# Kernel optimization log

Hardware: AMD Instinct MI355X
Metric: run time of the kernel (lower is better)

## Reference

```python
import jax, jax.numpy as jnp
import numpy as np

WINDOW = 5  # window_size
HALF = WINDOW // 2


def setup_inputs() -> dict:
    key = jax.random.key(0)
    k_x, k_w1, k_w2, k_b2 = jax.random.split(key, 4)
    N, D, D1, D2 = 200000, 320, 10, 5
    x = jax.random.normal(k_x, (N, D), dtype=jnp.float32)
    # torch Linear default init ~ U(-1/sqrt(fan_in), 1/sqrt(fan_in))
    W1 = jax.random.uniform(k_w1, (D1, D), dtype=jnp.float32, minval=-1, maxval=1) / np.sqrt(D)
    W2 = jax.random.uniform(k_w2, (D2, D1), dtype=jnp.float32, minval=-1, maxval=1) / np.sqrt(D1)
    b2 = jax.random.uniform(k_b2, (D2,), dtype=jnp.float32, minval=-1, maxval=1) / np.sqrt(D1)
    return {"x": x, "W1": W1, "W2": W2, "b2": b2}


def reference(x, W1, W2, b2):
    # linear1 (no bias) -> relu  (dropout is identity at inference)
    h = jax.nn.relu(x @ W1.T)                      # [N, dim1]
    # linear2 (+bias) -> (dropout identity) -> relu
    t = jax.nn.relu(h @ W2.T + b2)                 # [N, dim2]
    N, C = t.shape
    # zero-padded sliding window of size 5 over rows, fused gather
    padded = jnp.pad(t, ((HALF, HALF), (0, 0)))    # [N+4, C]
    win = jnp.stack([padded[k:k + N] for k in range(WINDOW)], axis=1)  # [N, 5, C]
    return win.reshape(N, WINDOW * C)              # [N, 25]
```

## Files before the change

### kernel.cpp

```cpp
#include <hip/hip_runtime.h>

#define D4    80
#define DIM1  10
#define DIM2  5
#define BLK   256
#define RPI   8
#define ITERS 10
#define CROWS (RPI * ITERS)
#define OROWS (CROWS - 4)

typedef float __attribute__((ext_vector_type(4))) f32x4;

__device__ __forceinline__ float row16_sum(float v) {
    int p;
    p = __builtin_amdgcn_update_dpp(0, __float_as_int(v), 0x128, 0xF, 0xF, true);
    v += __int_as_float(p);
    p = __builtin_amdgcn_update_dpp(0, __float_as_int(v), 0x124, 0xF, 0xF, true);
    v += __int_as_float(p);
    p = __builtin_amdgcn_update_dpp(0, __float_as_int(v), 0x122, 0xF, 0xF, true);
    v += __int_as_float(p);
    p = __builtin_amdgcn_update_dpp(0, __float_as_int(v), 0x121, 0xF, 0xF, true);
    v += __int_as_float(p);
    return v;
}

__global__ __launch_bounds__(BLK, 2)
void fused_fcl_win(const f32x4* __restrict__ x4,
                   const f32x4* __restrict__ w1g,
                   const float* __restrict__ w2,
                   const float* __restrict__ b2,
                   float*       __restrict__ out,
                   int N)
{
    __shared__ float t_lds[CROWS * DIM2];

    const int tid  = threadIdx.x;
    const int lane = tid & 63;
    const int wave = tid >> 6;
    const int s    = lane & 15;
    const int half = (lane >> 4) & 1;
    const int slot = wave * 2 + (lane >> 5);

    f32x4 w1r[5][5];
    {
        const f32x4* wp = w1g + (half * 5) * D4 + s;
        #pragma unroll
        for (int dd = 0; dd < 5; ++dd)
            #pragma unroll
            for (int i = 0; i < 5; ++i)
                w1r[dd][i] = wp[dd * D4 + i * 16];
    }

    const int j = (s < DIM2) ? s : 0;
    float w2h[5];
    #pragma unroll
    for (int dd = 0; dd < 5; ++dd)
        w2h[dd] = w2[j * DIM1 + half * 5 + dd];
    const float b2r = b2[j];

    const int base = (int)blockIdx.x * OROWS;

    auto loadrow = [&](int it, f32x4* xv) {
        int r  = base - 2 + it * RPI + slot;
        int rc = min(max(r, 0), N - 1);
        const f32x4* xp = x4 + (size_t)rc * D4 + s;
        #pragma unroll
        for (int i = 0; i < 5; ++i)
            xv[i] = __builtin_nontemporal_load(xp + i * 16);
    };

    f32x4 xv[5];
    loadrow(0, xv);

    for (int it = 0; it < ITERS; ++it) {
        f32x4 xn[5];
        if (it + 1 < ITERS) loadrow(it + 1, xn);

        float partial = 0.f;
        #pragma unroll
        for (int dd = 0; dd < 5; ++dd) {
            float acc = 0.f;
            #pragma unroll
            for (int i = 0; i < 5; ++i) {
                f32x4 a  = w1r[dd][i];
                f32x4 xx = xv[i];
                acc += xx.x * a.x; acc += xx.y * a.y;
                acc += xx.z * a.z; acc += xx.w * a.w;
            }
            acc = row16_sum(acc);
            partial += fmaxf(acc, 0.f) * w2h[dd];
        }
        const float other = __shfl_xor(partial, 16);
        float t5 = fmaxf(b2r + partial + other, 0.f);

        const int r = base - 2 + it * RPI + slot;
        if (r < 0 || r >= N) t5 = 0.f;
        if (half == 0 && s < DIM2)
            t_lds[(it * RPI + slot) * DIM2 + s] = t5;

        #pragma unroll
        for (int i = 0; i < 5; ++i) xv[i] = xn[i];
    }
    __syncthreads();

    const int lim = min(OROWS, N - base);
    const int nf  = lim * 25;
    float*    ob  = out + (size_t)base * 25;
    const int nf4 = nf >> 2;
    for (int f = tid; f < nf4; f += BLK) {
        int e   = f * 4;
        int nr  = e / 25;
        int c   = e - nr * 25;
        int idx = nr * 5 + c;
        float v[4];
        #pragma unroll
        for (int u = 0; u < 4; ++u) {
            v[u] = t_lds[idx];
            ++c; ++idx;
            if (c == 25) { c = 0; idx -= 20; }
        }
        f32x4 vv = { v[0], v[1], v[2], v[3] };
        __builtin_nontemporal_store(vv, (f32x4*)(ob + e));
    }
    for (int e = (nf & ~3) + tid; e < nf; e += BLK) {
        int nr = e / 25;
        ob[e] = t_lds[e - 20 * nr];
    }
}

extern "C" void kernel_launch(void* const* d_in, const int* in_sizes, int n_in,
                              void* d_out, int out_size, void* d_ws, size_t ws_size,
                              hipStream_t stream)
{
    const f32x4* x4 = (const f32x4*)d_in[0];
    const f32x4* w1 = (const f32x4*)d_in[1];
    const float* w2 = (const float*)d_in[2];
    const float* b2 = (const float*)d_in[3];

    const int N = in_sizes[0] / 320;
    float* out = (float*)d_out;

    const int grid = (N + OROWS - 1) / OROWS;
    fused_fcl_win<<<grid, BLK, 0, stream>>>(x4, w1, w2, b2, out, N);
}
```

Baseline: 56.80 us.

## Give each 16-lane group a full row, spill part of W1 to LDS

Each 16-lane group now computes all ten hidden units for its own row, rather than splitting them across two half-waves and combining with a cross-lane shuffle. Four W1 rows stay in registers and the other six are staged in shared memory. This frees registers so occupancy can rise to three blocks per SM, and it doubles the rows handled per iteration and per block. The cost is more LDS reads of weights in the inner loop and twice the arithmetic per lane, since halves no longer share work.

```diff
diff --git a/kernel.cpp b/kernel.cpp
--- a/kernel.cpp
+++ b/kernel.cpp
@@ -4,10 +4,12 @@
 #define DIM1  10
 #define DIM2  5
 #define BLK   256
-#define RPI   8
+#define RPI   16
 #define ITERS 10
 #define CROWS (RPI * ITERS)
 #define OROWS (CROWS - 4)
+#define NREG  4
+#define NLDS  (DIM1 - NREG)
 
 typedef float __attribute__((ext_vector_type(4))) f32x4;
 
@@ -24,7 +26,11 @@
     return v;
 }
 
-__global__ __launch_bounds__(BLK, 2)
+__device__ __forceinline__ float dot4(f32x4 a, f32x4 b) {
+    return a.x * b.x + a.y * b.y + a.z * b.z + a.w * b.w;
+}
+
+__global__ __launch_bounds__(BLK, 3)
 void fused_fcl_win(const f32x4* __restrict__ x4,
                    const f32x4* __restrict__ w1g,
                    const float* __restrict__ w2,
@@ -32,31 +38,33 @@
                    float*       __restrict__ out,
                    int N)
 {
+    __shared__ f32x4 w1s[NLDS * D4];
     __shared__ float t_lds[CROWS * DIM2];
 
     const int tid  = threadIdx.x;
     const int lane = tid & 63;
     const int wave = tid >> 6;
     const int s    = lane & 15;
-    const int half = (lane >> 4) & 1;
-    const int slot = wave * 2 + (lane >> 5);
+    const int g    = lane >> 4;
+    const int slot = wave * 4 + g;
 
-    f32x4 w1r[5][5];
-    {
-        const f32x4* wp = w1g + (half * 5) * D4 + s;
+    for (int f = tid; f < NLDS * D4; f += BLK)
+        w1s[f] = w1g[NREG * D4 + f];
+
+    f32x4 w1r[NREG][5];
+    #pragma unroll
+    for (int dd = 0; dd < NREG; ++dd)
         #pragma unroll
-        for (int dd = 0; dd < 5; ++dd)
-            #pragma unroll
-            for (int i = 0; i < 5; ++i)
-                w1r[dd][i] = wp[dd * D4 + i * 16];
-    }
+        for (int i = 0; i < 5; ++i)
+            w1r[dd][i] = w1g[dd * D4 + s + 16 * i];
 
     const int j = (s < DIM2) ? s : 0;
-    float w2h[5];
+    float w2r[DIM1];
     #pragma unroll
-    for (int dd = 0; dd < 5; ++dd)
-        w2h[dd] = w2[j * DIM1 + half * 5 + dd];
+    for (int d = 0; d < DIM1; ++d) w2r[d] = w2[j * DIM1 + d];
     const float b2r = b2[j];
+
+    __syncthreads();
 
     const int base = (int)blockIdx.x * OROWS;
 
@@ -72,30 +80,38 @@
     f32x4 xv[5];
     loadrow(0, xv);
 
+    int wofs = 0;
     for (int it = 0; it < ITERS; ++it) {
         f32x4 xn[5];
         if (it + 1 < ITERS) loadrow(it + 1, xn);
 
-        float partial = 0.f;
+        asm volatile("" : "+v"(wofs));
+
+        float partial = b2r;
         #pragma unroll
-        for (int dd = 0; dd < 5; ++dd) {
+        for (int dd = 0; dd < NREG; ++dd) {
+            float acc = 0.f;
+            #pragma unroll
+            for (int i = 0; i < 5; ++i) acc += dot4(w1r[dd][i], xv[i]);
+            acc = row16_sum(acc);
+            partial += fmaxf(acc, 0.f) * w2r[dd];
+        }
+        #pragma unroll
+        for (int dd = 0; dd < NLDS; ++dd) {
             float acc = 0.f;
             #pragma unroll
             for (int i = 0; i < 5; ++i) {
-                f32x4 a  = w1r[dd][i];
-                f32x4 xx = xv[i];
-                acc += xx.x * a.x; acc += xx.y * a.y;
-                acc += xx.z * a.z; acc += xx.w * a.w;
+                f32x4 w = w1s[wofs + dd * D4 + s + 16 * i];
+                acc += dot4(w, xv[i]);
             }
             acc = row16_sum(acc);
-            partial += fmaxf(acc, 0.f) * w2h[dd];
+            partial += fmaxf(acc, 0.f) * w2r[NREG + dd];
         }
-        const float other = __shfl_xor(partial, 16);
-        float t5 = fmaxf(b2r + partial + other, 0.f);
+        float t5 = fmaxf(partial, 0.f);
 
         const int r = base - 2 + it * RPI + slot;
         if (r < 0 || r >= N) t5 = 0.f;
-        if (half == 0 && s < DIM2)
+        if (s < DIM2)
             t_lds[(it * RPI + slot) * DIM2 + s] = t5;
 
         #pragma unroll
```

Result: no change. 56.70 us (-0.2%).
